# Performance work log

Measured on AMD Instinct MI355X. Metric: run time of the kernel, lower is better.

The kernel has to match this reference:

```python
import jax, jax.numpy as jnp
import numpy as np

C_CLIP = 10.0  # Bello et al. logit clipping constant (init arg C)


def setup_inputs() -> dict:
    key = jax.random.key(0)
    k1, k2, k3, k4, k5 = jax.random.split(key, 5)
    B, S, D = 64, 2048, 512
    scale = 1.0 / np.sqrt(D)  # ~torch Linear default init scale
    src = jax.random.normal(k1, (B, S, D), dtype=jnp.float32)
    tgt = jax.random.normal(k2, (B, 1, D), dtype=jnp.float32)
    W_q = jax.random.normal(k3, (D, D), dtype=jnp.float32) * scale
    W_ref = jax.random.normal(k4, (D, D), dtype=jnp.float32) * scale
    v = jax.random.uniform(k5, (D,), dtype=jnp.float32)  # uniform_(0, 1) as in source
    return {"src": src, "tgt": tgt, "W_q": W_q, "W_ref": W_ref, "v": v}


def reference(src, tgt, W_q, W_ref, v):
    # h = tanh(W_q(tgt) + W_ref(src))  -> [B, S, D] (tgt broadcasts over S)
    h = jnp.tanh(tgt @ W_q.T + src @ W_ref.T)
    # u = bmm(v, h^T) -> [B, 1, S]
    u = jnp.einsum("bsd,d->bs", h, v)[:, None, :]
    # logit clipping: C * tanh(u)
    logit = C_CLIP * jnp.tanh(u)
    probs = jax.nn.softmax(logit, axis=-1)  # [B, 1, S]
    # d_prime = bmm(probs, src) -> [B, 1, D]  ('Sup' path glimpse)
    d_prime = jnp.einsum("bqs,bsd->bqd", probs, src)
    return (d_prime, probs, logit)
```

## Files before the change

### kernel.cpp

```cpp
#include <hip/hip_runtime.h>
#include <math.h>

#define NB 64
#define NS 2048
#define ND 512
#define MTOT (NB * NS)
#define CCLIP 10.0f

typedef _Float16 f16x8 __attribute__((ext_vector_type(8)));
typedef _Float16 f16x4 __attribute__((ext_vector_type(4)));
typedef float f32x4 __attribute__((ext_vector_type(4)));

__device__ __forceinline__ void gl2lds16(const void* g, void* l) {
  __builtin_amdgcn_global_load_lds(
      (const __attribute__((address_space(1))) void*)(uintptr_t)g,
      (__attribute__((address_space(3))) void*)(uintptr_t)l, 16, 0, 0);
}

__device__ __forceinline__ float tanh_fast(float x) {
  float e = __expf(2.f * x);
  return 1.f - 2.f * __builtin_amdgcn_rcpf(e + 1.f);
}

__global__ __launch_bounds__(256) void cvtw_kernel(
    const float4* __restrict__ w4, _Float16* __restrict__ WhA) {
  const int idx = blockIdx.x * 256 + threadIdx.x;
  const int d = idx >> 7;
  const int k = (idx & 127) << 2;
  float4 x = w4[idx];
  f16x4 o;
  o[0] = (_Float16)x.x; o[1] = (_Float16)x.y;
  o[2] = (_Float16)x.z; o[3] = (_Float16)x.w;
  const int kt = k >> 5;
  const int kg = (k >> 3) & 3;
  const int h = k & 7;
  *(f16x4*)(WhA + ((size_t)((kt * 4 + kg) * 512 + d) * 8 + h)) = o;
}

__global__ __launch_bounds__(256) void qk_kernel(const float* __restrict__ tgt,
                                                 const float* __restrict__ Wq,
                                                 float* __restrict__ q_ws) {
  const int b = blockIdx.x >> 1;
  const int d = ((blockIdx.x & 1) << 8) + threadIdx.x;
  __shared__ float tl[ND];
  tl[threadIdx.x] = tgt[b * ND + threadIdx.x];
  tl[threadIdx.x + 256] = tgt[b * ND + threadIdx.x + 256];
  __syncthreads();
  const float4* wr = (const float4*)(Wq + (size_t)d * ND);
  float acc = 0.f;
#pragma unroll 8
  for (int k4 = 0; k4 < ND / 4; ++k4) {
    float4 w4 = wr[k4];
    acc += w4.x * tl[4 * k4 + 0] + w4.y * tl[4 * k4 + 1] +
           w4.z * tl[4 * k4 + 2] + w4.w * tl[4 * k4 + 3];
  }
  q_ws[b * ND + d] = acc;
}

__global__ __launch_bounds__(256, 2) void gemm_kernel(
    const float* __restrict__ src, const _Float16* __restrict__ WhA,
    const float* __restrict__ q_ws, const float* __restrict__ v,
    float* __restrict__ out_logit, float* __restrict__ out_probs_w) {
  __shared__ __align__(16) _Float16 sA[4 * 64 * 8];
  __shared__ __align__(16) _Float16 sB[4 * 512 * 8];
  __shared__ float ured[4 * 64];

  const int tid = threadIdx.x;
  const int lane = tid & 63;
  const int w = tid >> 6;
  const int s0 = blockIdx.x << 6;
  const int bb = blockIdx.x >> 5;

  const int quad = lane >> 4;
  const int l15 = lane & 15;

  const int ar = tid & 63;
  const int akg = tid >> 6;
  const float4* ap =
      (const float4*)(src + ((size_t)(s0 + ar) << 9)) + akg * 2;
  _Float16* aw = sA + (akg * 64 + ar) * 8;

  const char* gB = (const char*)WhA;

  f32x4 acc[4][8];
#pragma unroll
  for (int i = 0; i < 4; ++i)
#pragma unroll
    for (int j = 0; j < 8; ++j) acc[i][j] = (f32x4){0.f, 0.f, 0.f, 0.f};

  for (int kt = 0; kt < 16; ++kt) {
    __syncthreads();
#pragma unroll
    for (int i = 0; i < 8; ++i) {
      const int c = w * 8 + i;
      gl2lds16(gB + (size_t)kt * 32768 + c * 1024 + lane * 16,
               (char*)sB + c * 1024);
    }
    float4 x0 = ap[kt * 8];
    float4 x1 = ap[kt * 8 + 1];
    f16x8 h;
    h[0] = (_Float16)x0.x; h[1] = (_Float16)x0.y;
    h[2] = (_Float16)x0.z; h[3] = (_Float16)x0.w;
    h[4] = (_Float16)x1.x; h[5] = (_Float16)x1.y;
    h[6] = (_Float16)x1.z; h[7] = (_Float16)x1.w;
    *(f16x8*)aw = h;
    __syncthreads();

    f16x8 af[4], bf[8];
#pragma unroll
    for (int i = 0; i < 4; ++i)
      af[i] = *(const f16x8*)(sA + (quad * 64 + 16 * i + l15) * 8);
#pragma unroll
    for (int j = 0; j < 8; ++j)
      bf[j] = *(const f16x8*)(sB + (quad * 512 + w * 128 + 16 * j + l15) * 8);
#pragma unroll
    for (int i = 0; i < 4; ++i)
#pragma unroll
      for (int j = 0; j < 8; ++j)
        acc[i][j] = __builtin_amdgcn_mfma_f32_16x16x32_f16(af[i], bf[j],
                                                           acc[i][j], 0, 0, 0);
  }

  float pu[4][4];
#pragma unroll
  for (int i = 0; i < 4; ++i)
#pragma unroll
    for (int r = 0; r < 4; ++r) pu[i][r] = 0.f;

#pragma unroll
  for (int j = 0; j < 8; ++j) {
    const int dl = w * 128 + 16 * j + l15;
    const float qq = q_ws[bb * ND + dl];
    const float vv = v[dl];
#pragma unroll
    for (int i = 0; i < 4; ++i) {
      f32x4 a = acc[i][j];
#pragma unroll
      for (int r = 0; r < 4; ++r) pu[i][r] += tanh_fast(a[r] + qq) * vv;
    }
  }

#pragma unroll
  for (int i = 0; i < 4; ++i)
#pragma unroll
    for (int r = 0; r < 4; ++r) {
      float x = pu[i][r];
      x += __shfl_xor(x, 1, 16);
      x += __shfl_xor(x, 2, 16);
      x += __shfl_xor(x, 4, 16);
      x += __shfl_xor(x, 8, 16);
      pu[i][r] = x;
    }

  if (l15 == 0) {
#pragma unroll
    for (int i = 0; i < 4; ++i)
#pragma unroll
      for (int r = 0; r < 4; ++r)
        ured[w * 64 + 16 * i + quad * 4 + r] = pu[i][r];
  }
  __syncthreads();
  if (tid < 64) {
    const float u =
        ured[tid] + ured[64 + tid] + ured[128 + tid] + ured[192 + tid];
    const float lg = CCLIP * tanhf(u);
    out_logit[s0 + tid] = lg;
    out_probs_w[s0 + tid] = expf(lg - CCLIP);
  }
}

__global__ __launch_bounds__(256) void dp_kernel(const float* __restrict__ src,
                                                 const float* __restrict__ w_ws,
                                                 float* __restrict__ dp_ws) {
  const int blk = blockIdx.x;
  const int b = blk >> 4;
  const int ch = (blk >> 1) & 7;
  const int half = blk & 1;
  const int tid = threadIdx.x;
  const int row0 = b * NS + ch * 256;
  const float* base = src + ((size_t)row0 << 9) + (half << 8) + tid;
  float a = 0.f;
#pragma unroll 8
  for (int s = 0; s < 256; ++s) a += w_ws[row0 + s] * base[(size_t)s << 9];
  dp_ws[(size_t)blk * 256 + tid] = a;
}

__global__ __launch_bounds__(256) void fin_kernel(
    const float* __restrict__ dp_ws, float* __restrict__ out_dp,
    float* __restrict__ out_probs) {
  const int b = blockIdx.x;
  const int tid = threadIdx.x;
  __shared__ float red[4];
  __shared__ float s_inv;

  float x = 0.f;
  for (int idx = tid; idx < NS; idx += 256) x += out_probs[b * NS + idx];
#pragma unroll
  for (int m = 32; m; m >>= 1) x += __shfl_xor(x, m, 64);
  if ((tid & 63) == 0) red[tid >> 6] = x;
  __syncthreads();
  if (tid == 0) s_inv = 1.f / (red[0] + red[1] + red[2] + red[3]);
  __syncthreads();
  const float inv = s_inv;

  for (int idx = tid; idx < NS; idx += 256)
    out_probs[b * NS + idx] *= inv;

  for (int d = tid; d < ND; d += 256) {
    const int half = d >> 8;
    const int dl = d & 255;
    float acc = 0.f;
#pragma unroll
    for (int ch = 0; ch < 8; ++ch)
      acc += dp_ws[(size_t)(((b * 8 + ch) << 1) + half) * 256 + dl];
    out_dp[b * ND + d] = acc * inv;
  }
}

extern "C" void kernel_launch(void* const* d_in, const int* in_sizes, int n_in,
                              void* d_out, int out_size, void* d_ws,
                              size_t ws_size, hipStream_t stream) {
  const float* src = (const float*)d_in[0];
  const float* tgt = (const float*)d_in[1];
  const float* Wq = (const float*)d_in[2];
  const float* Wref = (const float*)d_in[3];
  const float* v = (const float*)d_in[4];

  float* out = (float*)d_out;
  float* out_dp = out;
  float* out_probs = out + NB * ND;
  float* out_logit = out + NB * ND + NB * NS;

  char* ws = (char*)d_ws;
  _Float16* WhA = (_Float16*)ws;
  float* q_ws = (float*)(ws + 524288);
  float* dp_ws = (float*)(ws + 655360);

  cvtw_kernel<<<256, 256, 0, stream>>>((const float4*)Wref, WhA);
  qk_kernel<<<2 * NB, 256, 0, stream>>>(tgt, Wq, q_ws);
  gemm_kernel<<<MTOT / 64, 256, 0, stream>>>(src, WhA, q_ws, v, out_logit,
                                             out_probs);
  dp_kernel<<<NB * 16, 256, 0, stream>>>(src, out_probs, dp_ws);
  fin_kernel<<<NB, 256, 0, stream>>>(dp_ws, out_dp, out_probs);
}
```

Measured before the change: 480.9 us.

## Double-buffer GEMM LDS tiles with register prefetch and vectorize dp reduction

The GEMM kernel now double-buffers its A and B LDS tiles. It prefetches src two k-tiles ahead into registers and issues the next B tile's global-to-LDS loads before the current MFMAs, which leaves one barrier per iteration instead of two. This is meant to overlap global load latency with compute, at the cost of doubled LDS and dropping the 2-blocks-per-SM launch bound, which can lower occupancy. The dp kernel is reorganized so each thread reads float4 rows across full D in 128-row chunks with a shared-memory partial sum, and fin_kernel is adapted to 16 chunks.

```diff
diff --git a/kernel.cpp b/kernel.cpp
--- a/kernel.cpp
+++ b/kernel.cpp
@@ -20,6 +20,15 @@
 __device__ __forceinline__ float tanh_fast(float x) {
   float e = __expf(2.f * x);
   return 1.f - 2.f * __builtin_amdgcn_rcpf(e + 1.f);
+}
+
+__device__ __forceinline__ f16x8 cvt8(float4 a, float4 b) {
+  f16x8 h;
+  h[0] = (_Float16)a.x; h[1] = (_Float16)a.y;
+  h[2] = (_Float16)a.z; h[3] = (_Float16)a.w;
+  h[4] = (_Float16)b.x; h[5] = (_Float16)b.y;
+  h[6] = (_Float16)b.z; h[7] = (_Float16)b.w;
+  return h;
 }
 
 __global__ __launch_bounds__(256) void cvtw_kernel(
@@ -57,12 +66,12 @@
   q_ws[b * ND + d] = acc;
 }
 
-__global__ __launch_bounds__(256, 2) void gemm_kernel(
+__global__ __launch_bounds__(256) void gemm_kernel(
     const float* __restrict__ src, const _Float16* __restrict__ WhA,
     const float* __restrict__ q_ws, const float* __restrict__ v,
     float* __restrict__ out_logit, float* __restrict__ out_probs_w) {
-  __shared__ __align__(16) _Float16 sA[4 * 64 * 8];
-  __shared__ __align__(16) _Float16 sB[4 * 512 * 8];
+  __shared__ __align__(16) _Float16 sA[2][4 * 64 * 8];
+  __shared__ __align__(16) _Float16 sB[2][4 * 512 * 8];
   __shared__ float ured[4 * 64];
 
   const int tid = threadIdx.x;
@@ -70,17 +79,24 @@
   const int w = tid >> 6;
   const int s0 = blockIdx.x << 6;
   const int bb = blockIdx.x >> 5;
-
   const int quad = lane >> 4;
   const int l15 = lane & 15;
 
   const int ar = tid & 63;
   const int akg = tid >> 6;
-  const float4* ap =
-      (const float4*)(src + ((size_t)(s0 + ar) << 9)) + akg * 2;
-  _Float16* aw = sA + (akg * 64 + ar) * 8;
-
+  const float4* ap = (const float4*)(src + ((size_t)(s0 + ar) << 9)) + akg * 2;
+  const int awoff = (akg * 64 + ar) * 8;
   const char* gB = (const char*)WhA;
+  const int bco = w * 8192 + lane * 16;
+
+  float4 xa[2][2];
+  xa[0][0] = ap[0]; xa[0][1] = ap[1];
+  xa[1][0] = ap[8]; xa[1][1] = ap[9];
+#pragma unroll
+  for (int i = 0; i < 8; ++i)
+    gl2lds16(gB + bco + i * 1024, (char*)sB[0] + bco + i * 1024);
+  *(f16x8*)(sA[0] + awoff) = cvt8(xa[0][0], xa[0][1]);
+  __syncthreads();
 
   f32x4 acc[4][8];
 #pragma unroll
@@ -88,37 +104,36 @@
 #pragma unroll
     for (int j = 0; j < 8; ++j) acc[i][j] = (f32x4){0.f, 0.f, 0.f, 0.f};
 
+#pragma unroll
   for (int kt = 0; kt < 16; ++kt) {
-    __syncthreads();
-#pragma unroll
-    for (int i = 0; i < 8; ++i) {
-      const int c = w * 8 + i;
-      gl2lds16(gB + (size_t)kt * 32768 + c * 1024 + lane * 16,
-               (char*)sB + c * 1024);
-    }
-    float4 x0 = ap[kt * 8];
-    float4 x1 = ap[kt * 8 + 1];
-    f16x8 h;
-    h[0] = (_Float16)x0.x; h[1] = (_Float16)x0.y;
-    h[2] = (_Float16)x0.z; h[3] = (_Float16)x0.w;
-    h[4] = (_Float16)x1.x; h[5] = (_Float16)x1.y;
-    h[6] = (_Float16)x1.z; h[7] = (_Float16)x1.w;
-    *(f16x8*)aw = h;
-    __syncthreads();
-
+    const int cur = kt & 1;
+    const int nxt = cur ^ 1;
+    if (kt + 2 < 16) {
+      xa[cur][0] = ap[(kt + 2) * 8];
+      xa[cur][1] = ap[(kt + 2) * 8 + 1];
+    }
+    if (kt + 1 < 16) {
+#pragma unroll
+      for (int i = 0; i < 8; ++i)
+        gl2lds16(gB + (size_t)(kt + 1) * 32768 + bco + i * 1024,
+                 (char*)sB[nxt] + bco + i * 1024);
+      *(f16x8*)(sA[nxt] + awoff) = cvt8(xa[nxt][0], xa[nxt][1]);
+    }
     f16x8 af[4], bf[8];
 #pragma unroll
     for (int i = 0; i < 4; ++i)
-      af[i] = *(const f16x8*)(sA + (quad * 64 + 16 * i + l15) * 8);
+      af[i] = *(const f16x8*)(sA[cur] + (quad * 64 + 16 * i + l15) * 8);
 #pragma unroll
     for (int j = 0; j < 8; ++j)
-      bf[j] = *(const f16x8*)(sB + (quad * 512 + w * 128 + 16 * j + l15) * 8);
+      bf[j] =
+          *(const f16x8*)(sB[cur] + (quad * 512 + w * 128 + 16 * j + l15) * 8);
 #pragma unroll
     for (int i = 0; i < 4; ++i)
 #pragma unroll
       for (int j = 0; j < 8; ++j)
         acc[i][j] = __builtin_amdgcn_mfma_f32_16x16x32_f16(af[i], bf[j],
                                                            acc[i][j], 0, 0, 0);
+    __syncthreads();
   }
 
   float pu[4][4];
@@ -172,17 +187,31 @@
 __global__ __launch_bounds__(256) void dp_kernel(const float* __restrict__ src,
                                                  const float* __restrict__ w_ws,
                                                  float* __restrict__ dp_ws) {
+  __shared__ float4 part[128];
   const int blk = blockIdx.x;
   const int b = blk >> 4;
-  const int ch = (blk >> 1) & 7;
-  const int half = blk & 1;
+  const int ch = blk & 15;
   const int tid = threadIdx.x;
-  const int row0 = b * NS + ch * 256;
-  const float* base = src + ((size_t)row0 << 9) + (half << 8) + tid;
-  float a = 0.f;
+  const int row0 = b * NS + ch * 128;
+  const int c4 = (tid & 127) << 2;
+  const int ro = tid >> 7;
+  const float4* base =
+      (const float4*)(src + ((size_t)(row0 + ro) << 9) + c4);
+  const float* wp = w_ws + row0 + ro;
+  float4 a = {0.f, 0.f, 0.f, 0.f};
 #pragma unroll 8
-  for (int s = 0; s < 256; ++s) a += w_ws[row0 + s] * base[(size_t)s << 9];
-  dp_ws[(size_t)blk * 256 + tid] = a;
+  for (int s = 0; s < 64; ++s) {
+    const float wv = wp[2 * s];
+    const float4 x = base[(size_t)s * 256];
+    a.x += wv * x.x; a.y += wv * x.y; a.z += wv * x.z; a.w += wv * x.w;
+  }
+  if (ro == 1) part[tid & 127] = a;
+  __syncthreads();
+  if (ro == 0) {
+    const float4 p = part[tid];
+    a.x += p.x; a.y += p.y; a.z += p.z; a.w += p.w;
+    *(float4*)(dp_ws + (size_t)blk * ND + c4) = a;
+  }
 }
 
 __global__ __launch_bounds__(256) void fin_kernel(
@@ -207,12 +236,10 @@
     out_probs[b * NS + idx] *= inv;
 
   for (int d = tid; d < ND; d += 256) {
-    const int half = d >> 8;
-    const int dl = d & 255;
     float acc = 0.f;
 #pragma unroll
-    for (int ch = 0; ch < 8; ++ch)
-      acc += dp_ws[(size_t)(((b * 8 + ch) << 1) + half) * 256 + dl];
+    for (int ch = 0; ch < 16; ++ch)
+      acc += dp_ws[(size_t)(b * 16 + ch) * ND + d];
     out_dp[b * ND + d] = acc * inv;
   }
 }
```

Result: slower. 533.2 us (+10.9%).
